# Performance work log

Measured on AMD Instinct MI355X. Metric: run time of the kernel, lower is better.

## Reference

```python
import jax, jax.numpy as jnp
import numpy as np

N = 262144   # active voxels
C = 128      # channels (in == out)
B, Z, Y, X = 2, 41, 512, 512
EPS = 1e-3   # BN eps from norm_cfg


def _build_neighbors():
    """Build submanifold rulebook-style neighbor tables along z, y, x axes.
    Each table is [N, 3] (offsets -1, 0, +1); missing neighbor -> sentinel N
    (points at a zero-padded feature row)."""
    rng = np.random.default_rng(0)
    total = B * Z * Y * X
    lin = np.sort(rng.choice(total, size=N, replace=False)).astype(np.int64)
    lookup = np.full(total, -1, dtype=np.int64)
    lookup[lin] = np.arange(N)
    r = lin % (Z * Y * X)
    z = r // (Y * X)
    r2 = r % (Y * X)
    y = r2 // X
    x = r2 % X

    def nbrs(axis_vals, axis_size, stride):
        cols = []
        for off in (-1, 0, 1):
            v = axis_vals + off
            valid = (v >= 0) & (v < axis_size)
            nlin = np.clip(lin + off * stride, 0, total - 1)
            idx = np.where(valid, lookup[nlin], -1)
            idx = np.where(idx < 0, N, idx)
            cols.append(idx)
        return np.stack(cols, axis=1).astype(np.int32)

    return nbrs(z, Z, Y * X), nbrs(y, Y, X), nbrs(x, X, 1)


def setup_inputs() -> dict:
    key = jax.random.key(0)
    ks = jax.random.split(key, 8)
    nbr_z, nbr_y, nbr_x = _build_neighbors()
    scale = 1.0 / np.sqrt(3 * C)
    inp = {
        "features": jax.random.normal(ks[0], (N, C), dtype=jnp.float32),
        "W1": jax.random.normal(ks[1], (3, C, C), dtype=jnp.float32) * scale,  # conv3x1x1
        "W2": jax.random.normal(ks[2], (3, C, C), dtype=jnp.float32) * scale,  # conv1x3x1
        "W3": jax.random.normal(ks[3], (3, C, C), dtype=jnp.float32) * scale,  # conv1x1x3
        "g0": jax.random.normal(ks[4], (C,), dtype=jnp.float32) * 0.1 + 1.0,
        "b0": jnp.zeros((C,), dtype=jnp.float32),
        "m0": jax.random.normal(ks[5], (C,), dtype=jnp.float32) * 0.1,
        "v0": jax.random.uniform(ks[5], (C,), minval=0.5, maxval=1.5, dtype=jnp.float32),
        "g2": jax.random.normal(ks[6], (C,), dtype=jnp.float32) * 0.1 + 1.0,
        "b2": jnp.zeros((C,), dtype=jnp.float32),
        "m2": jax.random.normal(ks[6], (C,), dtype=jnp.float32) * 0.1,
        "v2": jax.random.uniform(ks[6], (C,), minval=0.5, maxval=1.5, dtype=jnp.float32),
        "g3": jax.random.normal(ks[7], (C,), dtype=jnp.float32) * 0.1 + 1.0,
        "b3": jnp.zeros((C,), dtype=jnp.float32),
        "m3": jax.random.normal(ks[7], (C,), dtype=jnp.float32) * 0.1,
        "v3": jax.random.uniform(ks[7], (C,), minval=0.5, maxval=1.5, dtype=jnp.float32),
        "nbr_z": jnp.asarray(nbr_z),
        "nbr_y": jnp.asarray(nbr_y),
        "nbr_x": jnp.asarray(nbr_x),
    }
    return inp


def _subm_conv(feats, nbr, W):
    # submanifold gather-matmul: out[n] = sum_k W[k] @ feats[nbr[n,k]] (sentinel -> 0)
    feats_pad = jnp.concatenate([feats, jnp.zeros((1, feats.shape[1]), feats.dtype)], axis=0)
    gathered = feats_pad[nbr]  # [N, 3, C]
    return jnp.einsum('nkc,kcd->nd', gathered, W)


def _bn(x, g, b, m, v):
    return (x - m) * (g * jax.lax.rsqrt(v + EPS)) + b


def reference(features, W1, W2, W3, g0, b0, m0, v0, g2, b2, m2, v2,
              g3, b3, m3, v3, nbr_z, nbr_y, nbr_x):
    # Branch 1: conv3x1x1 -> bn0 -> sigmoid, then (source bug) bn0_2 -> sigmoid applied again
    s = jax.nn.sigmoid(_bn(_subm_conv(features, nbr_z, W1), g0, b0, m0, v0))
    s = jax.nn.sigmoid(_bn(s, g2, b2, m2, v2))
    # Branch 2: conv1x3x1, added raw (its BN/act were mistakenly applied to branch 1)
    s2 = _subm_conv(features, nbr_y, W2)
    # Branch 3: conv1x1x3 -> bn0_3 -> sigmoid
    s3 = jax.nn.sigmoid(_bn(_subm_conv(features, nbr_x, W3), g3, b3, m3, v3))
    return (s + s2 + s3) * features
```

## Files before the change

kernel.cpp:

```cpp
#include <hip/hip_runtime.h>
#include <hip/hip_bf16.h>
#include <stdint.h>
#include <stddef.h>

#define NVOX 262144
#define CCH 128
#define BN_EPS 1e-3f

typedef __attribute__((ext_vector_type(8))) short bfrag;
typedef __attribute__((ext_vector_type(4))) float f4;

#define AS1 __attribute__((address_space(1)))
#define AS3 __attribute__((address_space(3)))

__device__ __forceinline__ unsigned short f2bf(float f) {
  union { float f; unsigned u; } v; v.f = f;
  unsigned r = v.u + 0x7fffu + ((v.u >> 16) & 1u);
  return (unsigned short)(r >> 16);
}

__device__ __forceinline__ bfrag pack8(f4 x, f4 y) {
  bfrag r;
  r[0] = (short)f2bf(x[0]); r[1] = (short)f2bf(x[1]);
  r[2] = (short)f2bf(x[2]); r[3] = (short)f2bf(x[3]);
  r[4] = (short)f2bf(y[0]); r[5] = (short)f2bf(y[1]);
  r[6] = (short)f2bf(y[2]); r[7] = (short)f2bf(y[3]);
  return r;
}

__device__ __forceinline__ float sigmoidf_(float x) {
  const float e = __builtin_amdgcn_exp2f(x * -1.44269504f);
  return __builtin_amdgcn_rcpf(1.f + e);
}

__device__ __forceinline__ float bf2f(unsigned short h) {
  union { unsigned u; float f; } v; v.u = ((unsigned)h) << 16; return v.f;
}

__global__ void prep_wfrag(const float* __restrict__ W1, const float* __restrict__ W2,
                           const float* __restrict__ W3, unsigned short* __restrict__ wf) {
  const int frag = blockIdx.x;
  const int tile = frag & 7;
  const int kc   = (frag >> 3) & 3;
  const int tap  = (frag >> 5) % 3;
  const int conv = frag / 96;
  const float* W = (conv == 0) ? W1 : ((conv == 1) ? W2 : W3);
  const int l   = threadIdx.x;
  const int col = tile * 16 + (l & 15);
  const int k0  = kc * 32 + (l >> 4) * 8;
  bfrag o;
#pragma unroll
  for (int e = 0; e < 8; ++e)
    o[e] = (short)f2bf(W[(size_t)(tap * CCH + k0 + e) * CCH + col]);
  *reinterpret_cast<bfrag*>(wf + (size_t)frag * 512 + l * 8) = o;
}

__global__ void prep_bn(const float* g0, const float* b0, const float* m0, const float* v0,
                        const float* g2, const float* b2, const float* m2, const float* v2,
                        const float* g3, const float* b3, const float* m3, const float* v3,
                        float* __restrict__ bn) {
  const int c = threadIdx.x;
  const float s0 = g0[c] * rsqrtf(v0[c] + BN_EPS);
  const float s2 = g2[c] * rsqrtf(v2[c] + BN_EPS);
  const float s3 = g3[c] * rsqrtf(v3[c] + BN_EPS);
  bn[0 * CCH + c] = s0; bn[1 * CCH + c] = b0[c] - m0[c] * s0;
  bn[2 * CCH + c] = s2; bn[3 * CCH + c] = b2[c] - m2[c] * s2;
  bn[4 * CCH + c] = s3; bn[5 * CCH + c] = b3[c] - m3[c] * s3;
}

__global__ void prep_bf16(const float* __restrict__ feats, unsigned short* __restrict__ fbf) {
  const size_t base = ((size_t)blockIdx.x * 256 + threadIdx.x) * 8;
  const f4 x = *reinterpret_cast<const f4*>(feats + base);
  const f4 y = *reinterpret_cast<const f4*>(feats + base + 4);
  *reinterpret_cast<bfrag*>(fbf + base) = pack8(x, y);
  if (blockIdx.x == 0 && threadIdx.x < 16) {
    bfrag z = {0, 0, 0, 0, 0, 0, 0, 0};
    *reinterpret_cast<bfrag*>(fbf + (size_t)NVOX * CCH + threadIdx.x * 8) = z;
  }
}

__global__ __launch_bounds__(512, 4)
void recon_v17(const unsigned short* __restrict__ fbf,
               const unsigned short* __restrict__ wfrag,
               const float* __restrict__ bn,
               const int* __restrict__ nbrz, const int* __restrict__ nbrx,
               const int* __restrict__ nbry,
               float* __restrict__ out) {
  __shared__ unsigned short Bb[24576];

  const int tid  = threadIdx.x;
  const int lane = tid & 63;
  const int w    = tid >> 6;
  const int l15  = lane & 15;
  const int lhi  = lane >> 4;
  const int cb   = blockIdx.x & 1;
  const int row0 = (blockIdx.x >> 1) * 128;
  const int wrow = row0 + w * 16;

  auto fillconv = [&](int RB) {
#pragma unroll
    for (int i = 0; i < 6; ++i) {
      const int L    = w * 6 + i;
      const int slot = L >> 4;
      const int sub  = L & 15;
      const int g    = ((RB + slot) * 4 + (sub >> 2)) * 8 + cb * 4 + (sub & 3);
      __builtin_amdgcn_global_load_lds(
          (const AS1 void*)(wfrag + (size_t)g * 512 + lane * 8),
          (AS3 void*)((char*)Bb + L * 1024), 16, 0, 0);
    }
  };

  fillconv(0);
  const int row = wrow + l15;
  const int rg  = row * 3;
  const int izp = nbrz[rg + 0], izn = nbrz[rg + 2];
  const int ixp = nbrx[rg + 0], ixn = nbrx[rg + 2];
  const int iyp = nbry[rg + 0], iyn = nbry[rg + 2];

  const bool azp = __any(izp != NVOX), azn = __any(izn != NVOX);
  const bool axp = __any(ixp != NVOX), axn = __any(ixn != NVOX);
  const bool ayp = __any(iyp != NVOX), ayn = __any(iyn != NVOX);

  bfrag aF[4];
  bfrag aS[4];

#define LOADF(DST, IDX) {                                                     \
    const char* p = (const char*)fbf + ((size_t)(unsigned)(IDX) << 8) + (lhi << 4); \
    DST[0] = *reinterpret_cast<const bfrag*>(p);                              \
    DST[1] = *reinterpret_cast<const bfrag*>(p + 64);                         \
    DST[2] = *reinterpret_cast<const bfrag*>(p + 128);                        \
    DST[3] = *reinterpret_cast<const bfrag*>(p + 192);                        \
  }

#define TAP(SLOT, AFR, ACCS) {                                                \
    const char* bs = (const char*)Bb + (SLOT) * 16384 + lane * 16;            \
    _Pragma("unroll")                                                         \
    for (int kc = 0; kc < 4; ++kc) {                                          \
      _Pragma("unroll")                                                       \
      for (int ct = 0; ct < 4; ++ct) {                                        \
        const bfrag b = *reinterpret_cast<const bfrag*>(                      \
            bs + (kc * 4 + ct) * 1024);                                       \
        ACCS[ct] = __builtin_amdgcn_mfma_f32_16x16x32_bf16(                   \
            AFR[kc], b, ACCS[ct], 0, 0, 0);                                   \
      } } }

#define CONV(VP, VN, IP, IN, ACCS)                                            \
  {                                                                           \
    if (VP)      LOADF(aF, IP)                                                \
    else if (VN) LOADF(aF, IN)                                                \
    TAP(1, aS, ACCS)                                                          \
    if (VP) {                                                                 \
      TAP(0, aF, ACCS)                                                        \
      if (VN) { LOADF(aF, IN)  TAP(2, aF, ACCS) }                             \
    } else if (VN) {                                                          \
      TAP(2, aF, ACCS)                                                        \
    }                                                                         \
  }

  LOADF(aS, row)

  __syncthreads();

  f4 acc[4], run[4];
#pragma unroll
  for (int ct = 0; ct < 4; ++ct) {
    acc[ct] = f4{0.f, 0.f, 0.f, 0.f};
    run[ct] = f4{0.f, 0.f, 0.f, 0.f};
  }

  CONV(azp, azn, izp, izn, acc)
  __syncthreads();
  fillconv(6);
#pragma unroll
  for (int ct = 0; ct < 4; ++ct) {
    const int col = cb * 64 + ct * 16 + l15;
    const float sc0 = bn[0 * CCH + col], sh0 = bn[1 * CCH + col];
    const float sc2 = bn[2 * CCH + col], sh2 = bn[3 * CCH + col];
#pragma unroll
    for (int j = 0; j < 4; ++j) {
      const float u = sigmoidf_(sc0 * acc[ct][j] + sh0);
      run[ct][j] = sigmoidf_(sc2 * u + sh2);
    }
    acc[ct] = f4{0.f, 0.f, 0.f, 0.f};
  }
  __syncthreads();

  CONV(axp, axn, ixp, ixn, acc)
  __syncthreads();
  fillconv(3);
#pragma unroll
  for (int ct = 0; ct < 4; ++ct) {
    const int col = cb * 64 + ct * 16 + l15;
    const float sc3 = bn[4 * CCH + col], sh3 = bn[5 * CCH + col];
#pragma unroll
    for (int j = 0; j < 4; ++j)
      run[ct][j] += sigmoidf_(sc3 * acc[ct][j] + sh3);
  }
  __syncthreads();

  CONV(ayp, ayn, iyp, iyn, run)

#undef CONV
#undef TAP
#undef LOADF

#pragma unroll
  for (int ct = 0; ct < 4; ++ct) {
    const int col = cb * 64 + ct * 16 + l15;
#pragma unroll
    for (int j = 0; j < 4; ++j) {
      const int r = wrow + (lhi << 2) + j;
      const size_t o = ((size_t)r << 7) + col;
      out[o] = run[ct][j] * bf2f(fbf[o]);
    }
  }
}

__global__ void recon_naive(const float* __restrict__ feats,
    const float* __restrict__ W1, const float* __restrict__ W2, const float* __restrict__ W3,
    const int* __restrict__ nbrz, const int* __restrict__ nbry, const int* __restrict__ nbrx,
    const float* g0, const float* b0, const float* m0, const float* v0,
    const float* g2, const float* b2, const float* m2, const float* v2,
    const float* g3, const float* b3, const float* m3, const float* v3,
    float* __restrict__ out) {
  __shared__ float rows[3][CCH];
  const int n = blockIdx.x;
  const int d = threadIdx.x;
  float res[3];
#pragma unroll
  for (int conv = 0; conv < 3; ++conv) {
    const int* nbr  = (conv == 0) ? nbrz : ((conv == 1) ? nbry : nbrx);
    const float* W  = (conv == 0) ? W1 : ((conv == 1) ? W2 : W3);
#pragma unroll
    for (int tap = 0; tap < 3; ++tap) {
      const int idx = nbr[n * 3 + tap];
      rows[tap][d] = ((unsigned)idx < (unsigned)NVOX) ? feats[((size_t)idx << 7) + d] : 0.f;
    }
    __syncthreads();
    const float* rflat = &rows[0][0];
    float s = 0.f;
    for (int k = 0; k < 3 * CCH; ++k) s += rflat[k] * W[(size_t)k * CCH + d];
    res[conv] = s;
    __syncthreads();
  }
  const float sc0 = g0[d] * rsqrtf(v0[d] + BN_EPS), sh0 = b0[d] - m0[d] * sc0;
  const float sc2 = g2[d] * rsqrtf(v2[d] + BN_EPS), sh2 = b2[d] - m2[d] * sc2;
  const float sc3 = g3[d] * rsqrtf(v3[d] + BN_EPS), sh3 = b3[d] - m3[d] * sc3;
  float u = 1.f / (1.f + __expf(-(sc0 * res[0] + sh0)));
  u = 1.f / (1.f + __expf(-(sc2 * u + sh2)));
  const float s3v = 1.f / (1.f + __expf(-(sc3 * res[2] + sh3)));
  out[((size_t)n << 7) + d] = (u + res[1] + s3v) * feats[((size_t)n << 7) + d];
}

extern "C" void kernel_launch(void* const* d_in, const int* in_sizes, int n_in,
                              void* d_out, int out_size, void* d_ws, size_t ws_size,
                              hipStream_t stream) {
  const float* feats = (const float*)d_in[0];
  const float* W1 = (const float*)d_in[1];
  const float* W2 = (const float*)d_in[2];
  const float* W3 = (const float*)d_in[3];
  const float* g0 = (const float*)d_in[4];
  const float* b0 = (const float*)d_in[5];
  const float* m0 = (const float*)d_in[6];
  const float* v0 = (const float*)d_in[7];
  const float* g2 = (const float*)d_in[8];
  const float* b2 = (const float*)d_in[9];
  const float* m2 = (const float*)d_in[10];
  const float* v2 = (const float*)d_in[11];
  const float* g3 = (const float*)d_in[12];
  const float* b3 = (const float*)d_in[13];
  const float* m3 = (const float*)d_in[14];
  const float* v3 = (const float*)d_in[15];
  const int* nz = (const int*)d_in[16];
  const int* ny = (const int*)d_in[17];
  const int* nx = (const int*)d_in[18];
  float* out = (float*)d_out;

  const size_t wf_bytes = 288u * 1024u;
  const size_t bn_bytes = 4096u;
  const size_t fb_bytes = ((size_t)NVOX + 1) * CCH * sizeof(short);
  if (ws_size >= wf_bytes + bn_bytes + fb_bytes) {
    unsigned short* wf  = (unsigned short*)d_ws;
    float*          bnt = (float*)((char*)d_ws + wf_bytes);
    unsigned short* fbf = (unsigned short*)((char*)d_ws + wf_bytes + bn_bytes);
    hipLaunchKernelGGL(prep_wfrag, dim3(288), dim3(64), 0, stream, W1, W2, W3, wf);
    hipLaunchKernelGGL(prep_bn, dim3(1), dim3(CCH), 0, stream,
                       g0, b0, m0, v0, g2, b2, m2, v2, g3, b3, m3, v3, bnt);
    hipLaunchKernelGGL(prep_bf16, dim3((NVOX * CCH) / (256 * 8)), dim3(256), 0, stream,
                       feats, fbf);
    hipLaunchKernelGGL(recon_v17, dim3((NVOX / 128) * 2), dim3(512), 0, stream,
                       fbf, wf, bnt, nz, nx, ny, out);
  } else {
    hipLaunchKernelGGL(recon_naive, dim3(NVOX), dim3(CCH), 0, stream,
                       feats, W1, W2, W3, nz, ny, nx,
                       g0, b0, m0, v0, g2, b2, m2, v2, g3, b3, m3, v3, out);
  }
}
```

Before: 140.7 us.

## Read weight fragments directly from global memory instead of staging through LDS

Removes the shared-memory weight buffer, the global_load_lds fills and all block barriers; each wave now loads B fragments for every MFMA straight from global memory, where the shared weight table should stay cache-resident. Blocks shrink from 512 to 256 threads (64 rows each) and the launch bound changes to allow more blocks per CU. The intent is to cut barrier stalls and LDS traffic. In exchange every wave issues its own global weight loads, with more latency and L2/L1 bandwidth pressure per MFMA.

```diff
diff --git a/kernel.cpp b/kernel.cpp
--- a/kernel.cpp
+++ b/kernel.cpp
@@ -9,9 +9,6 @@
 
 typedef __attribute__((ext_vector_type(8))) short bfrag;
 typedef __attribute__((ext_vector_type(4))) float f4;
-
-#define AS1 __attribute__((address_space(1)))
-#define AS3 __attribute__((address_space(3)))
 
 __device__ __forceinline__ unsigned short f2bf(float f) {
   union { float f; unsigned u; } v; v.f = f;
@@ -79,38 +76,22 @@
   }
 }
 
-__global__ __launch_bounds__(512, 4)
-void recon_v17(const unsigned short* __restrict__ fbf,
+__global__ __launch_bounds__(256, 6)
+void recon_v18(const unsigned short* __restrict__ fbf,
                const unsigned short* __restrict__ wfrag,
                const float* __restrict__ bn,
                const int* __restrict__ nbrz, const int* __restrict__ nbrx,
                const int* __restrict__ nbry,
                float* __restrict__ out) {
-  __shared__ unsigned short Bb[24576];
-
   const int tid  = threadIdx.x;
   const int lane = tid & 63;
   const int w    = tid >> 6;
   const int l15  = lane & 15;
   const int lhi  = lane >> 4;
   const int cb   = blockIdx.x & 1;
-  const int row0 = (blockIdx.x >> 1) * 128;
+  const int row0 = (blockIdx.x >> 1) * 64;
   const int wrow = row0 + w * 16;
 
-  auto fillconv = [&](int RB) {
-#pragma unroll
-    for (int i = 0; i < 6; ++i) {
-      const int L    = w * 6 + i;
-      const int slot = L >> 4;
-      const int sub  = L & 15;
-      const int g    = ((RB + slot) * 4 + (sub >> 2)) * 8 + cb * 4 + (sub & 3);
-      __builtin_amdgcn_global_load_lds(
-          (const AS1 void*)(wfrag + (size_t)g * 512 + lane * 8),
-          (AS3 void*)((char*)Bb + L * 1024), 16, 0, 0);
-    }
-  };
-
-  fillconv(0);
   const int row = wrow + l15;
   const int rg  = row * 3;
   const int izp = nbrz[rg + 0], izn = nbrz[rg + 2];
@@ -132,34 +113,33 @@
     DST[3] = *reinterpret_cast<const bfrag*>(p + 192);                        \
   }
 
-#define TAP(SLOT, AFR, ACCS) {                                                \
-    const char* bs = (const char*)Bb + (SLOT) * 16384 + lane * 16;            \
+#define TAP(REGION, AFR, ACCS) {                                              \
+    const unsigned short* bs = wfrag + (size_t)(REGION) * 16384               \
+                               + (cb << 11) + lane * 8;                       \
     _Pragma("unroll")                                                         \
     for (int kc = 0; kc < 4; ++kc) {                                          \
       _Pragma("unroll")                                                       \
       for (int ct = 0; ct < 4; ++ct) {                                        \
         const bfrag b = *reinterpret_cast<const bfrag*>(                      \
-            bs + (kc * 4 + ct) * 1024);                                       \
+            bs + kc * 4096 + ct * 512);                                       \
         ACCS[ct] = __builtin_amdgcn_mfma_f32_16x16x32_bf16(                   \
             AFR[kc], b, ACCS[ct], 0, 0, 0);                                   \
       } } }
 
-#define CONV(VP, VN, IP, IN, ACCS)                                            \
+#define CONV(VP, VN, IP, IN, RP, RS, RN, ACCS)                                \
   {                                                                           \
     if (VP)      LOADF(aF, IP)                                                \
     else if (VN) LOADF(aF, IN)                                                \
-    TAP(1, aS, ACCS)                                                          \
+    TAP(RS, aS, ACCS)                                                         \
     if (VP) {                                                                 \
-      TAP(0, aF, ACCS)                                                        \
-      if (VN) { LOADF(aF, IN)  TAP(2, aF, ACCS) }                             \
+      TAP(RP, aF, ACCS)                                                       \
+      if (VN) { LOADF(aF, IN)  TAP(RN, aF, ACCS) }                            \
     } else if (VN) {                                                          \
-      TAP(2, aF, ACCS)                                                        \
+      TAP(RN, aF, ACCS)                                                       \
     }                                                                         \
   }
 
   LOADF(aS, row)
-
-  __syncthreads();
 
   f4 acc[4], run[4];
 #pragma unroll
@@ -168,9 +148,7 @@
     run[ct] = f4{0.f, 0.f, 0.f, 0.f};
   }
 
-  CONV(azp, azn, izp, izn, acc)
-  __syncthreads();
-  fillconv(6);
+  CONV(azp, azn, izp, izn, 0, 1, 2, acc)
 #pragma unroll
   for (int ct = 0; ct < 4; ++ct) {
     const int col = cb * 64 + ct * 16 + l15;
@@ -183,11 +161,7 @@
     }
     acc[ct] = f4{0.f, 0.f, 0.f, 0.f};
   }
-  __syncthreads();
-
-  CONV(axp, axn, ixp, ixn, acc)
-  __syncthreads();
-  fillconv(3);
+  CONV(axp, axn, ixp, ixn, 6, 7, 8, acc)
 #pragma unroll
   for (int ct = 0; ct < 4; ++ct) {
     const int col = cb * 64 + ct * 16 + l15;
@@ -196,9 +170,7 @@
     for (int j = 0; j < 4; ++j)
       run[ct][j] += sigmoidf_(sc3 * acc[ct][j] + sh3);
   }
-  __syncthreads();
-
-  CONV(ayp, ayn, iyp, iyn, run)
+  CONV(ayp, ayn, iyp, iyn, 3, 4, 5, run)
 
 #undef CONV
 #undef TAP
@@ -288,7 +260,7 @@
                        g0, b0, m0, v0, g2, b2, m2, v2, g3, b3, m3, v3, bnt);
     hipLaunchKernelGGL(prep_bf16, dim3((NVOX * CCH) / (256 * 8)), dim3(256), 0, stream,
                        feats, fbf);
-    hipLaunchKernelGGL(recon_v17, dim3((NVOX / 128) * 2), dim3(512), 0, stream,
+    hipLaunchKernelGGL(recon_v18, dim3((NVOX / 64) * 2), dim3(256), 0, stream,
                        fbf, wf, bnt, nz, nx, ny, out);
   } else {
     hipLaunchKernelGGL(recon_naive, dim3(NVOX), dim3(CCH), 0, stream,
```

Measured after the change: 266.9 us. 1.9x slower.
